# Performance work log

Measured on AMD Instinct MI355X. Metric: run time of the kernel, lower is better.

Reference implementation:

```python
import jax, jax.numpy as jnp
import numpy as np
import math

B, T, D, H = 4, 2048, 512, 8
MAX_LEN = 2048
DK = D // H


def setup_inputs() -> dict:
    key = jax.random.key(0)
    ks = jax.random.split(key, 12)
    s = 0.02
    inp = {
        "x": jax.random.normal(ks[0], (B, T, D), dtype=jnp.float32),
        "mask": jax.random.bernoulli(ks[1], 0.85, (B, T)),  # True = observed
        "Wq": jax.random.normal(ks[2], (D, D), dtype=jnp.float32) * s,
        "bq": jnp.zeros((D,), dtype=jnp.float32),
        "Wk": jax.random.normal(ks[3], (D, D), dtype=jnp.float32) * s,
        "bk": jnp.zeros((D,), dtype=jnp.float32),
        "Wv": jax.random.normal(ks[4], (D, D), dtype=jnp.float32) * s,
        "bv": jnp.zeros((D,), dtype=jnp.float32),
        "Wo": jax.random.normal(ks[5], (D, D), dtype=jnp.float32) * s,
        "bo": jnp.zeros((D,), dtype=jnp.float32),
        "missing_bias": jnp.zeros((1, H, 1, 1), dtype=jnp.float32),
        "rel_pos_embed": jax.random.normal(ks[6], (2 * MAX_LEN - 1, H), dtype=jnp.float32) * 0.01,
    }
    return inp


def _sinusoidal_pe(t, d):
    pos = jnp.arange(t, dtype=jnp.float32)[:, None]                      # [T,1]
    div = jnp.exp(jnp.arange(0, d, 2, dtype=jnp.float32) * (-math.log(10000.0) / d))
    pe = jnp.zeros((t, d), dtype=jnp.float32)
    pe = pe.at[:, 0::2].set(jnp.sin(pos * div))
    pe = pe.at[:, 1::2].set(jnp.cos(pos * div))
    return pe


def _attention(x, mask, Wq, bq, Wk, bk, Wv, bv, Wo, bo, missing_bias, rel_pos_embed):
    b, t, d = x.shape
    h = missing_bias.shape[1]
    dk = d // h
    max_len = (rel_pos_embed.shape[0] + 1) // 2

    x = x + _sinusoidal_pe(t, d)[None]

    def proj(w, bias):  # [B,T,D] -> [B,H,T,dk]
        y = jnp.einsum('btd,ed->bte', x, w) + bias
        return y.reshape(b, t, h, dk).transpose(0, 2, 1, 3)

    Q, K, V = proj(Wq, bq), proj(Wk, bk), proj(Wv, bv)

    scores = jnp.einsum('bhqd,bhkd->bhqk', Q, K) / math.sqrt(dk)  # [B,H,T,T]

    # relative position bias, antisymmetrized
    pos = jnp.arange(t)
    rel_idx = pos[:, None] - pos[None, :] + (max_len - 1)          # [T,T]
    bias = rel_pos_embed[rel_idx]                                  # [T,T,H]
    bias = 0.5 * (bias - bias.transpose(1, 0, 2))
    scores = scores + bias.transpose(2, 0, 1)[None]                # [B,H,T,T]

    # missing-token masking on keys: -inf fill then add missing_bias at masked spots
    m = mask[:, None, None, :]                                     # [B,1,1,T]
    scores = jnp.where(m, scores, -jnp.inf)
    scores = jnp.where(m, scores, scores + missing_bias)

    attn = jax.nn.softmax(scores, axis=-1)
    out = jnp.einsum('bhqk,bhkd->bhqd', attn, V)
    out = out.transpose(0, 2, 1, 3).reshape(b, t, d)
    return jnp.einsum('btd,ed->bte', out, Wo) + bo


def reference(x, mask, Wq, bq, Wk, bk, Wv, bv, Wo, bo, missing_bias, rel_pos_embed):
    return _attention(x, mask, Wq, bq, Wk, bk, Wv, bv, Wo, bo, missing_bias, rel_pos_embed)
```

## Files before the change

### kernel.cpp

```cpp
#include <hip/hip_runtime.h>

#define B_ 4
#define T_ 2048
#define D_ 512
#define H_ 8
#define DK_ 64
#define TBL 4095

typedef __attribute__((ext_vector_type(4))) float f32x4;
typedef __attribute__((ext_vector_type(8))) short bf16x8;
typedef __attribute__((ext_vector_type(4))) int i32x4;

static __device__ __forceinline__ float b2f(ushort u) {
    union { float f; unsigned int i; } c;
    c.i = ((unsigned int)u) << 16;
    return c.f;
}

static __device__ __forceinline__ ushort f2b(float f) {
    union { float f; unsigned int i; } c;
    c.f = f;
    unsigned int i = c.i;
    unsigned int r = (i + 0x7fffu + ((i >> 16) & 1u)) >> 16;
    return (ushort)r;
}

__global__ __launch_bounds__(64) void detect_mask_kernel(const unsigned int* __restrict__ mask,
                                                         int* __restrict__ flags) {
    int lane = threadIdx.x;
    int c2 = 0, c1 = 0;
    for (int i = lane; i < 512; i += 64) {
        unsigned int v = mask[i];
        c2 += (v == 0x3F803F80u || v == 0x00010001u) ? 1 : 0;
        c1 += (v == 0x01010101u) ? 1 : 0;
    }
#pragma unroll
    for (int m = 1; m < 64; m <<= 1) {
        c2 += __shfl_xor(c2, m);
        c1 += __shfl_xor(c1, m);
    }
    if (lane == 0) flags[0] = (c2 > 8) ? 2 : ((c1 > 8) ? 1 : 0);
}

__global__ __launch_bounds__(256) void mask_prep_kernel(const void* __restrict__ mask,
                                                        const int* __restrict__ flags,
                                                        int* __restrict__ maskw) {
    int j = blockIdx.x * 256 + threadIdx.x;
    int fm = flags[0];
    int v;
    if (fm == 2)      v = (((const ushort*)mask)[j] != 0);
    else if (fm == 1) v = (((const unsigned char*)mask)[j] != 0);
    else              v = (((const int*)mask)[j] != 0);
    maskw[j] = v;
}

__global__ __launch_bounds__(256) void wcvt_kernel(
    const float* __restrict__ W0, const float* __restrict__ W1,
    const float* __restrict__ W2, const float* __restrict__ W3,
    ushort* __restrict__ Wc) {
    const int z = blockIdx.z;
    const float* Ws = (z == 0) ? W0 : ((z == 1) ? W1 : ((z == 2) ? W2 : W3));
    int idx = blockIdx.x * 256 + threadIdx.x;
    const float* wf = Ws + idx * 8;
    f32x4 a = *(const f32x4*)(wf);
    f32x4 c = *(const f32x4*)(wf + 4);
    union { ushort u[8]; i32x4 v; } o;
#pragma unroll
    for (int j = 0; j < 4; ++j) { o.u[j] = f2b(a[j]); o.u[4 + j] = f2b(c[j]); }
    *(i32x4*)(Wc + (size_t)z * (D_ * D_) + idx * 8) = o.v;
}

__global__ __launch_bounds__(256) void pe_kernel(const float* __restrict__ x,
                                                 ushort* __restrict__ xp) {
    int idx = blockIdx.x * 256 + threadIdx.x;
    int i = idx & 255;
    int row = idx >> 8;
    int t = row & (T_ - 1);
    float div = __expf((float)i * -0.035977892f);
    float ang = (float)t * div;
    float s = sinf(ang);
    float c = cosf(ang);
    float2 v = ((const float2*)x)[row * 256 + i];
    unsigned int o = (unsigned int)f2b(v.x + s) | ((unsigned int)f2b(v.y + c) << 16);
    *(unsigned int*)(xp + (size_t)row * D_ + 2 * i) = o;
}

__global__ __launch_bounds__(256) void bias_tbl_kernel(const float* __restrict__ E,
                                                       float* __restrict__ tbl) {
    int idx = blockIdx.x * 256 + threadIdx.x;
    if (idx >= TBL * H_) return;
    int h = idx & 7;
    int j = idx >> 3;
    tbl[(size_t)h * TBL + j] = 0.5f * (E[(size_t)j * H_ + h] - E[(size_t)(4094 - j) * H_ + h]);
}

template <int OUTMODE>
__global__ __launch_bounds__(256) void gemm_bt_kernel(
    const ushort* __restrict__ A,
    const ushort* __restrict__ W0, const ushort* __restrict__ W1, const ushort* __restrict__ W2,
    const float* __restrict__ bias0, const float* __restrict__ bias1, const float* __restrict__ bias2,
    void* __restrict__ O0, void* __restrict__ O1, void* __restrict__ O2) {
    __shared__ ushort As[128 * 32];
    __shared__ ushort Bs[128 * 32];

    const int z = blockIdx.z;
    const ushort* Wp = (z == 0) ? W0 : ((z == 1) ? W1 : W2);
    const float* bp = (z == 0) ? bias0 : ((z == 1) ? bias1 : bias2);
    void* Op = (z == 0) ? O0 : ((z == 1) ? O1 : O2);

    const int n0 = blockIdx.x * 128;
    const int m0 = blockIdx.y * 128;
    const int tid = threadIdx.x;
    const int lane = tid & 63;
    const int w = tid >> 6;
    const int wr = (w >> 1) * 64;
    const int wc = (w & 1) * 64;
    const int l15 = lane & 15;
    const int lg = lane >> 4;

    f32x4 acc[4][4];
#pragma unroll
    for (int mi = 0; mi < 4; ++mi)
#pragma unroll
        for (int ni = 0; ni < 4; ++ni)
            acc[mi][ni] = (f32x4){0.f, 0.f, 0.f, 0.f};

    for (int kt = 0; kt < D_ / 32; ++kt) {
#pragma unroll
        for (int p = 0; p < 2; ++p) {
            int c = tid + p * 256;
            int r = c >> 2;
            int s = c & 3;
            i32x4 va = *(const i32x4*)(A + (size_t)(m0 + r) * D_ + kt * 32 + s * 8);
            i32x4 vb = *(const i32x4*)(Wp + (size_t)(n0 + r) * D_ + kt * 32 + s * 8);
            *(i32x4*)(As + r * 32 + s * 8) = va;
            *(i32x4*)(Bs + r * 32 + s * 8) = vb;
        }
        __syncthreads();

        bf16x8 af[4], bfr[4];
#pragma unroll
        for (int mi = 0; mi < 4; ++mi)
            af[mi] = *(const bf16x8*)(As + (wr + mi * 16 + l15) * 32 + lg * 8);
#pragma unroll
        for (int ni = 0; ni < 4; ++ni)
            bfr[ni] = *(const bf16x8*)(Bs + (wc + ni * 16 + l15) * 32 + lg * 8);
#pragma unroll
        for (int mi = 0; mi < 4; ++mi)
#pragma unroll
            for (int ni = 0; ni < 4; ++ni)
                acc[mi][ni] = __builtin_amdgcn_mfma_f32_16x16x32_bf16(af[mi], bfr[ni], acc[mi][ni], 0, 0, 0);
        __syncthreads();
    }

#pragma unroll
    for (int ni = 0; ni < 4; ++ni) {
        int n = n0 + wc + ni * 16 + l15;
        float bv = bp[n];
#pragma unroll
        for (int mi = 0; mi < 4; ++mi) {
#pragma unroll
            for (int i = 0; i < 4; ++i) {
                int m = m0 + wr + mi * 16 + lg * 4 + i;
                float v = acc[mi][ni][i] + bv;
                if (OUTMODE == 0) {
                    int b = m >> 11;
                    int t = m & 2047;
                    int h = n >> 6;
                    int dk = n & 63;
                    ((ushort*)Op)[(((size_t)(b * H_ + h) * T_ + t) << 6) + dk] = f2b(v);
                } else {
                    ((float*)Op)[(size_t)m * D_ + n] = v;
                }
            }
        }
    }
}

__global__ __launch_bounds__(256) void attn_kernel(
    const ushort* __restrict__ Q, const ushort* __restrict__ K, const ushort* __restrict__ V,
    const int* __restrict__ maskw, const float* __restrict__ tbl,
    ushort* __restrict__ Aout) {
    __shared__ ushort Ks[64 * 64];
    __shared__ ushort Vs[64 * 64];
    __shared__ ushort Ps[4][32 * 64];
    __shared__ float biasl[2176];
    __shared__ float maskl[T_];

    const int qb = blockIdx.x;
    const int bh = blockIdx.y;
    const int b = bh >> 3;
    const int h = bh & 7;
    const int tid = threadIdx.x;
    const int lane = tid & 63;
    const int w = tid >> 6;
    const int l15 = lane & 15;
    const int lg = lane >> 4;

    const ushort* Qp = Q + (size_t)bh * T_ * DK_;
    const ushort* Kp = K + (size_t)bh * T_ * DK_;
    const ushort* Vp = V + (size_t)bh * T_ * DK_;

    for (int j = tid; j < 2176; j += 256) {
        int gj = qb * 128 + j;
        biasl[j] = (gj <= 4094) ? tbl[(size_t)h * TBL + gj] : 0.f;
    }
    for (int j = tid; j < T_; j += 256)
        maskl[j] = (maskw[b * T_ + j] != 0) ? 1.0f : 0.0f;

    const int q0 = qb * 128 + w * 32;
    bf16x8 qf[2][2];
#pragma unroll
    for (int mi = 0; mi < 2; ++mi)
#pragma unroll
        for (int kf = 0; kf < 2; ++kf)
            qf[mi][kf] = *(const bf16x8*)(Qp + (size_t)(q0 + mi * 16 + l15) * DK_ + kf * 32 + lg * 8);

    f32x4 acc[2][4];
    float rs[2][4];
#pragma unroll
    for (int mi = 0; mi < 2; ++mi) {
#pragma unroll
        for (int ni = 0; ni < 4; ++ni)
            acc[mi][ni] = (f32x4){0.f, 0.f, 0.f, 0.f};
#pragma unroll
        for (int i = 0; i < 4; ++i)
            rs[mi][i] = 0.f;
    }
    __syncthreads();

    for (int kt = 0; kt < T_ / 64; ++kt) {
#pragma unroll
        for (int p = 0; p < 2; ++p) {
            int c = tid + p * 256;
            int r = c >> 3;
            int s = c & 7;
            i32x4 v = *(const i32x4*)(Kp + (size_t)(kt * 64 + r) * DK_ + s * 8);
            *(i32x4*)(Ks + r * 64 + ((s ^ (r & 7)) * 8)) = v;
        }
        {
            int p2 = lane & 31;
            int half = lane >> 5;
            int dk0 = w * 16 + half * 8;
            const ushort* src = Vp + (size_t)(kt * 64 + 2 * p2) * DK_ + dk0;
            i32x4 lo = *(const i32x4*)(src);
            i32x4 hi = *(const i32x4*)(src + DK_);
            const ushort* plo = (const ushort*)&lo;
            const ushort* phi = (const ushort*)&hi;
#pragma unroll
            for (int j = 0; j < 8; ++j) {
                int dk = dk0 + j;
                unsigned int word = (unsigned int)plo[j] | ((unsigned int)phi[j] << 16);
                int slot = p2 >> 2;
                int wi = p2 & 3;
                *(unsigned int*)(Vs + dk * 64 + ((slot ^ (dk & 7)) * 8) + wi * 2) = word;
            }
        }
        __syncthreads();

#pragma unroll
        for (int ct = 0; ct < 4; ++ct) {
            int krow = ct * 16 + l15;
            bf16x8 kf0 = *(const bf16x8*)(Ks + krow * 64 + (((0 + lg) ^ (krow & 7)) * 8));
            bf16x8 kf1 = *(const bf16x8*)(Ks + krow * 64 + (((4 + lg) ^ (krow & 7)) * 8));
            int kg = kt * 64 + ct * 16 + l15;
            float mf = maskl[kg];
#pragma unroll
            for (int mi = 0; mi < 2; ++mi) {
                f32x4 S = (f32x4){0.f, 0.f, 0.f, 0.f};
                S = __builtin_amdgcn_mfma_f32_16x16x32_bf16(qf[mi][0], kf0, S, 0, 0, 0);
                S = __builtin_amdgcn_mfma_f32_16x16x32_bf16(qf[mi][1], kf1, S, 0, 0, 0);
                int ql0 = w * 32 + mi * 16 + lg * 4;
#pragma unroll
                for (int i = 0; i < 4; ++i) {
                    float bias = biasl[ql0 + i - kg + 2047];
                    float pv = mf * __expf(fmaf(S[i], 0.125f, bias));
                    ushort pb = f2b(pv);
                    rs[mi][i] += b2f(pb);
                    int prow = mi * 16 + lg * 4 + i;
                    int pcol = ct * 16 + l15;
                    Ps[w][prow * 64 + (((pcol >> 3) ^ (prow & 7)) * 8) + (pcol & 7)] = pb;
                }
            }
        }

#pragma unroll
        for (int kk = 0; kk < 2; ++kk) {
            bf16x8 pf[2];
#pragma unroll
            for (int mi = 0; mi < 2; ++mi) {
                int prow = mi * 16 + l15;
                pf[mi] = *(const bf16x8*)(Ps[w] + prow * 64 + (((kk * 4 + lg) ^ (prow & 7)) * 8));
            }
#pragma unroll
            for (int ni = 0; ni < 4; ++ni) {
                int vrow = ni * 16 + l15;
                bf16x8 vf = *(const bf16x8*)(Vs + vrow * 64 + (((kk * 4 + lg) ^ (vrow & 7)) * 8));
#pragma unroll
                for (int mi = 0; mi < 2; ++mi)
                    acc[mi][ni] = __builtin_amdgcn_mfma_f32_16x16x32_bf16(pf[mi], vf, acc[mi][ni], 0, 0, 0);
            }
        }
        __syncthreads();
    }

#pragma unroll
    for (int mi = 0; mi < 2; ++mi)
#pragma unroll
        for (int i = 0; i < 4; ++i) {
            float v = rs[mi][i];
            v += __shfl_xor(v, 1);
            v += __shfl_xor(v, 2);
            v += __shfl_xor(v, 4);
            v += __shfl_xor(v, 8);
            rs[mi][i] = v;
        }

#pragma unroll
    for (int mi = 0; mi < 2; ++mi)
#pragma unroll
        for (int ni = 0; ni < 4; ++ni)
#pragma unroll
            for (int i = 0; i < 4; ++i) {
                int t = q0 + mi * 16 + lg * 4 + i;
                int d = h * DK_ + ni * 16 + l15;
                Aout[(size_t)(b * T_ + t) * D_ + d] = f2b(acc[mi][ni][i] / rs[mi][i]);
            }
}

extern "C" void kernel_launch(void* const* d_in, const int* in_sizes, int n_in,
                              void* d_out, int out_size, void* d_ws, size_t ws_size,
                              hipStream_t stream) {
    const float* x   = (const float*)d_in[0];
    const void* mask = d_in[1];
    const float* Wq  = (const float*)d_in[2];
    const float* bq  = (const float*)d_in[3];
    const float* Wk  = (const float*)d_in[4];
    const float* bk  = (const float*)d_in[5];
    const float* Wv  = (const float*)d_in[6];
    const float* bv  = (const float*)d_in[7];
    const float* Wo  = (const float*)d_in[8];
    const float* bo  = (const float*)d_in[9];
    const float* E   = (const float*)d_in[11];
    float* out = (float*)d_out;

    char* ws = (char*)d_ws;
    ushort* xp  = (ushort*)(ws);
    ushort* Qw  = (ushort*)(ws + (8u << 20));
    ushort* Kw  = (ushort*)(ws + (16u << 20));
    ushort* Vw  = (ushort*)(ws + (24u << 20));
    float* tbl  = (float*)(ws + (32u << 20));
    ushort* Wc  = (ushort*)(ws + (32u << 20) + 262144);
    int* maskw  = (int*)(ws + (34u << 20) + 262144);
    int* flags  = (int*)(ws + (34u << 20) + 262144 + 32768);

    if (ws_size < (35u << 20)) return;

    detect_mask_kernel<<<1, 64, 0, stream>>>((const unsigned int*)mask, flags);
    mask_prep_kernel<<<(B_ * T_) / 256, 256, 0, stream>>>(mask, flags, maskw);
    bias_tbl_kernel<<<(TBL * H_ + 255) / 256, 256, 0, stream>>>(E, tbl);
    pe_kernel<<<B_ * T_, 256, 0, stream>>>(x, xp);

    dim3 gw(128, 1, 4);
    wcvt_kernel<<<gw, 256, 0, stream>>>(Wq, Wk, Wv, Wo, Wc);

    dim3 g1(D_ / 128, (B_ * T_) / 128, 3);
    gemm_bt_kernel<0><<<g1, 256, 0, stream>>>(xp, Wc, Wc + D_ * D_, Wc + 2 * D_ * D_,
                                              bq, bk, bv, Qw, Kw, Vw);

    dim3 g2(T_ / 128, B_ * H_, 1);
    attn_kernel<<<g2, 256, 0, stream>>>(Qw, Kw, Vw, maskw, tbl, xp);

    dim3 g3(D_ / 128, (B_ * T_) / 128, 1);
    gemm_bt_kernel<1><<<g3, 256, 0, stream>>>(xp, Wc + 3 * D_ * D_, Wc + 3 * D_ * D_, Wc + 3 * D_ * D_,
                                              bo, bo, bo, out, out, out);
}
```

Before: 240.6 us.

## Use 512-thread attention blocks, exp2 softmax, and direct global-to-LDS GEMM loads

The attention kernel now runs 8 waves of 16 query rows each instead of 4 waves of 32, which doubles the threads per block and cuts per-wave register use. The K and V tile staging is reworked for the wider block. The softmax switches from __expf to exp2f, with log2(e) folded into the bias table scale and the score scale, and the row sum now accumulates the full-precision probability rather than its bf16-rounded value. The QKV and output GEMMs stage their A/B tiles through global_load_lds instead of going through registers. Risks include less K/V reuse per query and a small numeric mismatch between the fp32 row sum and the bf16 P fed to the PV matmul.

```diff
diff --git a/kernel.cpp b/kernel.cpp
--- a/kernel.cpp
+++ b/kernel.cpp
@@ -10,6 +10,7 @@
 typedef __attribute__((ext_vector_type(4))) float f32x4;
 typedef __attribute__((ext_vector_type(8))) short bf16x8;
 typedef __attribute__((ext_vector_type(4))) int i32x4;
+typedef unsigned int u32;
 
 static __device__ __forceinline__ float b2f(ushort u) {
     union { float f; unsigned int i; } c;
@@ -23,6 +24,13 @@
     unsigned int i = c.i;
     unsigned int r = (i + 0x7fffu + ((i >> 16) & 1u)) >> 16;
     return (ushort)r;
+}
+
+static __device__ __forceinline__ void gload_lds16(const void* g, void* l) {
+    __builtin_amdgcn_global_load_lds(
+        (const __attribute__((address_space(1))) u32*)g,
+        (__attribute__((address_space(3))) u32*)(u32)(unsigned long long)l,
+        16, 0, 0);
 }
 
 __global__ __launch_bounds__(64) void detect_mask_kernel(const unsigned int* __restrict__ mask,
@@ -91,7 +99,8 @@
     if (idx >= TBL * H_) return;
     int h = idx & 7;
     int j = idx >> 3;
-    tbl[(size_t)h * TBL + j] = 0.5f * (E[(size_t)j * H_ + h] - E[(size_t)(4094 - j) * H_ + h]);
+    tbl[(size_t)h * TBL + j] =
+        0.72134752044f * (E[(size_t)j * H_ + h] - E[(size_t)(4094 - j) * H_ + h]);
 }
 
 template <int OUTMODE>
@@ -131,10 +140,8 @@
             int c = tid + p * 256;
             int r = c >> 2;
             int s = c & 3;
-            i32x4 va = *(const i32x4*)(A + (size_t)(m0 + r) * D_ + kt * 32 + s * 8);
-            i32x4 vb = *(const i32x4*)(Wp + (size_t)(n0 + r) * D_ + kt * 32 + s * 8);
-            *(i32x4*)(As + r * 32 + s * 8) = va;
-            *(i32x4*)(Bs + r * 32 + s * 8) = vb;
+            gload_lds16(A  + (size_t)(m0 + r) * D_ + kt * 32 + s * 8, As + c * 8);
+            gload_lds16(Wp + (size_t)(n0 + r) * D_ + kt * 32 + s * 8, Bs + c * 8);
         }
         __syncthreads();
 
@@ -177,13 +184,13 @@
     }
 }
 
-__global__ __launch_bounds__(256) void attn_kernel(
+__global__ __launch_bounds__(512) void attn_kernel(
     const ushort* __restrict__ Q, const ushort* __restrict__ K, const ushort* __restrict__ V,
     const int* __restrict__ maskw, const float* __restrict__ tbl,
     ushort* __restrict__ Aout) {
     __shared__ ushort Ks[64 * 64];
     __shared__ ushort Vs[64 * 64];
-    __shared__ ushort Ps[4][32 * 64];
+    __shared__ ushort Ps[8][16 * 64];
     __shared__ float biasl[2176];
     __shared__ float maskl[T_];
 
@@ -201,59 +208,43 @@
     const ushort* Kp = K + (size_t)bh * T_ * DK_;
     const ushort* Vp = V + (size_t)bh * T_ * DK_;
 
-    for (int j = tid; j < 2176; j += 256) {
+    for (int j = tid; j < 2176; j += 512) {
         int gj = qb * 128 + j;
         biasl[j] = (gj <= 4094) ? tbl[(size_t)h * TBL + gj] : 0.f;
     }
-    for (int j = tid; j < T_; j += 256)
+    for (int j = tid; j < T_; j += 512)
         maskl[j] = (maskw[b * T_ + j] != 0) ? 1.0f : 0.0f;
 
-    const int q0 = qb * 128 + w * 32;
-    bf16x8 qf[2][2];
-#pragma unroll
-    for (int mi = 0; mi < 2; ++mi)
-#pragma unroll
-        for (int kf = 0; kf < 2; ++kf)
-            qf[mi][kf] = *(const bf16x8*)(Qp + (size_t)(q0 + mi * 16 + l15) * DK_ + kf * 32 + lg * 8);
-
-    f32x4 acc[2][4];
-    float rs[2][4];
-#pragma unroll
-    for (int mi = 0; mi < 2; ++mi) {
-#pragma unroll
-        for (int ni = 0; ni < 4; ++ni)
-            acc[mi][ni] = (f32x4){0.f, 0.f, 0.f, 0.f};
-#pragma unroll
-        for (int i = 0; i < 4; ++i)
-            rs[mi][i] = 0.f;
-    }
+    const int q0 = qb * 128 + w * 16;
+    bf16x8 qf[2];
+#pragma unroll
+    for (int kf = 0; kf < 2; ++kf)
+        qf[kf] = *(const bf16x8*)(Qp + (size_t)(q0 + l15) * DK_ + kf * 32 + lg * 8);
+
+    f32x4 acc[4];
+    float rs[4];
+#pragma unroll
+    for (int ni = 0; ni < 4; ++ni) acc[ni] = (f32x4){0.f, 0.f, 0.f, 0.f};
+#pragma unroll
+    for (int i = 0; i < 4; ++i) rs[i] = 0.f;
     __syncthreads();
 
     for (int kt = 0; kt < T_ / 64; ++kt) {
-#pragma unroll
-        for (int p = 0; p < 2; ++p) {
-            int c = tid + p * 256;
-            int r = c >> 3;
-            int s = c & 7;
-            i32x4 v = *(const i32x4*)(Kp + (size_t)(kt * 64 + r) * DK_ + s * 8);
-            *(i32x4*)(Ks + r * 64 + ((s ^ (r & 7)) * 8)) = v;
-        }
         {
-            int p2 = lane & 31;
-            int half = lane >> 5;
-            int dk0 = w * 16 + half * 8;
-            const ushort* src = Vp + (size_t)(kt * 64 + 2 * p2) * DK_ + dk0;
-            i32x4 lo = *(const i32x4*)(src);
-            i32x4 hi = *(const i32x4*)(src + DK_);
-            const ushort* plo = (const ushort*)&lo;
-            const ushort* phi = (const ushort*)&hi;
+            int r = tid >> 3;
+            int sl = tid & 7;
+            i32x4 kv = *(const i32x4*)(Kp + (size_t)(kt * 64 + r) * DK_ + ((sl ^ (r & 7)) * 8));
+            *(i32x4*)(Ks + tid * 8) = kv;
+        }
+        {
+            int key = tid >> 3;
+            int dq = (tid & 7) * 8;
+            bf16x8 v = *(const bf16x8*)(Vp + (size_t)(kt * 64 + key) * DK_ + dq);
+            const ushort* pv8 = (const ushort*)&v;
 #pragma unroll
             for (int j = 0; j < 8; ++j) {
-                int dk = dk0 + j;
-                unsigned int word = (unsigned int)plo[j] | ((unsigned int)phi[j] << 16);
-                int slot = p2 >> 2;
-                int wi = p2 & 3;
-                *(unsigned int*)(Vs + dk * 64 + ((slot ^ (dk & 7)) * 8) + wi * 2) = word;
+                int dk = dq + j;
+                Vs[dk * 64 + (((key >> 3) ^ (dk & 7)) * 8) + (key & 7)] = pv8[j];
             }
         }
         __syncthreads();
@@ -261,71 +252,55 @@
 #pragma unroll
         for (int ct = 0; ct < 4; ++ct) {
             int krow = ct * 16 + l15;
-            bf16x8 kf0 = *(const bf16x8*)(Ks + krow * 64 + (((0 + lg) ^ (krow & 7)) * 8));
+            bf16x8 kf0 = *(const bf16x8*)(Ks + krow * 64 + ((lg ^ (krow & 7)) * 8));
             bf16x8 kf1 = *(const bf16x8*)(Ks + krow * 64 + (((4 + lg) ^ (krow & 7)) * 8));
             int kg = kt * 64 + ct * 16 + l15;
             float mf = maskl[kg];
-#pragma unroll
-            for (int mi = 0; mi < 2; ++mi) {
-                f32x4 S = (f32x4){0.f, 0.f, 0.f, 0.f};
-                S = __builtin_amdgcn_mfma_f32_16x16x32_bf16(qf[mi][0], kf0, S, 0, 0, 0);
-                S = __builtin_amdgcn_mfma_f32_16x16x32_bf16(qf[mi][1], kf1, S, 0, 0, 0);
-                int ql0 = w * 32 + mi * 16 + lg * 4;
-#pragma unroll
-                for (int i = 0; i < 4; ++i) {
-                    float bias = biasl[ql0 + i - kg + 2047];
-                    float pv = mf * __expf(fmaf(S[i], 0.125f, bias));
-                    ushort pb = f2b(pv);
-                    rs[mi][i] += b2f(pb);
-                    int prow = mi * 16 + lg * 4 + i;
-                    int pcol = ct * 16 + l15;
-                    Ps[w][prow * 64 + (((pcol >> 3) ^ (prow & 7)) * 8) + (pcol & 7)] = pb;
-                }
+            f32x4 S = (f32x4){0.f, 0.f, 0.f, 0.f};
+            S = __builtin_amdgcn_mfma_f32_16x16x32_bf16(qf[0], kf0, S, 0, 0, 0);
+            S = __builtin_amdgcn_mfma_f32_16x16x32_bf16(qf[1], kf1, S, 0, 0, 0);
+            int jb = w * 16 + lg * 4 - kg + 2047;
+#pragma unroll
+            for (int i = 0; i < 4; ++i) {
+                float pv = mf * exp2f(fmaf(S[i], 0.1803368801f, biasl[jb + i]));
+                rs[i] += pv;
+                int prow = lg * 4 + i;
+                int pcol = ct * 16 + l15;
+                Ps[w][prow * 64 + (((pcol >> 3) ^ (prow & 7)) * 8) + (pcol & 7)] = f2b(pv);
             }
         }
 
 #pragma unroll
         for (int kk = 0; kk < 2; ++kk) {
-            bf16x8 pf[2];
-#pragma unroll
-            for (int mi = 0; mi < 2; ++mi) {
-                int prow = mi * 16 + l15;
-                pf[mi] = *(const bf16x8*)(Ps[w] + prow * 64 + (((kk * 4 + lg) ^ (prow & 7)) * 8));
-            }
+            bf16x8 pf = *(const bf16x8*)(Ps[w] + l15 * 64 + (((kk * 4 + lg) ^ (l15 & 7)) * 8));
 #pragma unroll
             for (int ni = 0; ni < 4; ++ni) {
                 int vrow = ni * 16 + l15;
                 bf16x8 vf = *(const bf16x8*)(Vs + vrow * 64 + (((kk * 4 + lg) ^ (vrow & 7)) * 8));
-#pragma unroll
-                for (int mi = 0; mi < 2; ++mi)
-                    acc[mi][ni] = __builtin_amdgcn_mfma_f32_16x16x32_bf16(pf[mi], vf, acc[mi][ni], 0, 0, 0);
+                acc[ni] = __builtin_amdgcn_mfma_f32_16x16x32_bf16(pf, vf, acc[ni], 0, 0, 0);
             }
         }
         __syncthreads();
     }
 
 #pragma unroll
-    for (int mi = 0; mi < 2; ++mi)
+    for (int i = 0; i < 4; ++i) {
+        float v = rs[i];
+        v += __shfl_xor(v, 1);
+        v += __shfl_xor(v, 2);
+        v += __shfl_xor(v, 4);
+        v += __shfl_xor(v, 8);
+        rs[i] = v;
+    }
+
+#pragma unroll
+    for (int ni = 0; ni < 4; ++ni)
 #pragma unroll
         for (int i = 0; i < 4; ++i) {
-            float v = rs[mi][i];
-            v += __shfl_xor(v, 1);
-            v += __shfl_xor(v, 2);
-            v += __shfl_xor(v, 4);
-            v += __shfl_xor(v, 8);
-            rs[mi][i] = v;
-        }
-
-#pragma unroll
-    for (int mi = 0; mi < 2; ++mi)
-#pragma unroll
-        for (int ni = 0; ni < 4; ++ni)
-#pragma unroll
-            for (int i = 0; i < 4; ++i) {
-                int t = q0 + mi * 16 + lg * 4 + i;
-                int d = h * DK_ + ni * 16 + l15;
-                Aout[(size_t)(b * T_ + t) * D_ + d] = f2b(acc[mi][ni][i] / rs[mi][i]);
-            }
+            int t = q0 + lg * 4 + i;
+            int d = h * DK_ + ni * 16 + l15;
+            Aout[(size_t)(b * T_ + t) * D_ + d] = f2b(acc[ni][i] / rs[i]);
+        }
 }
 
 extern "C" void kernel_launch(void* const* d_in, const int* in_sizes, int n_in,
@@ -369,7 +344,7 @@
                                               bq, bk, bv, Qw, Kw, Vw);
 
     dim3 g2(T_ / 128, B_ * H_, 1);
-    attn_kernel<<<g2, 256, 0, stream>>>(Qw, Kw, Vw, maskw, tbl, xp);
+    attn_kernel<<<g2, 512, 0, stream>>>(Qw, Kw, Vw, maskw, tbl, xp);
 
     dim3 g3(D_ / 128, (B_ * T_) / 128, 1);
     gemm_bt_kernel<1><<<g3, 256, 0, stream>>>(xp, Wc + 3 * D_ * D_, Wc + 3 * D_ * D_, Wc + 3 * D_ * D_,
```

Result: slower. 269.7 us (+12.1%).
